# Kernel optimization log

Hardware: AMD Instinct MI355X
Metric: run time of the kernel (lower is better)

Reference implementation:

```python
import jax, jax.numpy as jnp
import numpy as np

B, S, D, H = 4, 2048, 128, 8

def setup_inputs() -> dict:
    key = jax.random.key(0)
    ks = jax.random.split(key, 11)
    sc_in = 1.0 / np.sqrt(D)
    sc_out = 1.0 / np.sqrt(H * D)
    return {
        "Q": jax.random.normal(ks[0], (B, S, D), jnp.float32),
        "K": jax.random.normal(ks[1], (B, S, D), jnp.float32),
        "V": jax.random.normal(ks[2], (B, S, D), jnp.float32),
        "WQ_w": jax.random.normal(ks[3], (H * D, D), jnp.float32) * sc_in,
        "WQ_b": jax.random.normal(ks[4], (H * D,), jnp.float32) * 0.01,
        "WK_w": jax.random.normal(ks[5], (H * D, D), jnp.float32) * sc_in,
        "WK_b": jax.random.normal(ks[6], (H * D,), jnp.float32) * 0.01,
        "WV_w": jax.random.normal(ks[7], (H * D, D), jnp.float32) * sc_in,
        "WV_b": jax.random.normal(ks[8], (H * D,), jnp.float32) * 0.01,
        "W_w": jax.random.normal(ks[9], (D, H * D), jnp.float32) * sc_out,
        "W_b": jax.random.normal(ks[10], (D,), jnp.float32) * 0.01,
    }

def reference(Q, K, V, WQ_w, WQ_b, WK_w, WK_b, WV_w, WV_b, W_w, W_b):
    b, s, d = Q.shape
    h = WQ_w.shape[0] // d
    # Linear projections: [b,s,d] -> [b,s,h*d] -> [b,h,s,d]
    rQ = (Q @ WQ_w.T + WQ_b).reshape(b, s, h, d).transpose(0, 2, 1, 3)
    rK = (K @ WK_w.T + WK_b).reshape(b, s, h, d).transpose(0, 2, 1, 3)
    rV = (V @ WV_w.T + WV_b).reshape(b, s, h, d).transpose(0, 2, 1, 3)
    # Scores: [b,h,s,s], scaled by sqrt(head_dim) = sqrt(input_dim)
    scores = jnp.einsum("bhqd,bhkd->bhqk", rQ, rK) / jnp.sqrt(jnp.asarray(d, rQ.dtype))
    sim = jax.nn.softmax(scores, axis=-1)
    # Attend and merge heads: [b,h,s,d] -> [b,s,h*d]
    oV = jnp.einsum("bhqk,bhkd->bqhd", sim, rV).reshape(b, s, h * d)
    return oV @ W_w.T + W_b
```

## Files before the change

### kernel.cpp

```cpp
#include <hip/hip_runtime.h>
#include <hip/hip_bf16.h>

typedef unsigned short u16;
typedef unsigned int   u32;
typedef short v8s __attribute__((ext_vector_type(8)));
typedef float v4f __attribute__((ext_vector_type(4)));
typedef float v16f __attribute__((ext_vector_type(16)));
typedef int   v2i __attribute__((ext_vector_type(2)));

#define MFMA16(a,b,c) __builtin_amdgcn_mfma_f32_16x16x32_bf16(a,b,c,0,0,0)
#define MFMA32(a,b,c) __builtin_amdgcn_mfma_f32_32x32x16_bf16(a,b,c,0,0,0)


__device__ __forceinline__ u16 f2b(float f){ u32 i; __builtin_memcpy(&i,&f,4); u32 r = (i + 0x7FFFu + ((i>>16)&1u))>>16; return (u16)r; }
__device__ __forceinline__ u32 pk2(float a, float b){
  __hip_bfloat162 h = __float22bfloat162_rn(make_float2(a,b));
  u32 r; __builtin_memcpy(&r,&h,4); return r;
}

__device__ __forceinline__ void gl16(const void* g, void* l){
  __builtin_amdgcn_global_load_lds((const __attribute__((address_space(1))) u32*)g,
                                   (__attribute__((address_space(3))) u32*)l, 16, 0, 0);
}

__device__ __forceinline__ void stage8f(const float* g, u16* l){
  float4 a = *(const float4*)g, b = *(const float4*)(g+4);
  uint4 q;
  q.x = pk2(a.x, a.y); q.y = pk2(a.z, a.w);
  q.z = pk2(b.x, b.y); q.w = pk2(b.z, b.w);
  *(uint4*)l = q;
}

__global__ __launch_bounds__(256) void proj_qkv(
    const float* __restrict__ Qx, const float* __restrict__ Kx, const float* __restrict__ Vx,
    const float* __restrict__ WQw, const float* __restrict__ WQb,
    const float* __restrict__ WKw, const float* __restrict__ WKb,
    const float* __restrict__ WVw, const float* __restrict__ WVb,
    u16* __restrict__ Qp, u16* __restrict__ Kp, u16* __restrict__ Vt)
{
  __shared__ u16 smem[32768];
  u16* As = smem;
  u16* Ws = smem + 16384;

  const int z = blockIdx.z;
  const float* X    = (z==0) ? Qx  : (z==1 ? Kx  : Vx);
  const float* W    = (z==0) ? WQw : (z==1 ? WKw : WVw);
  const float* bias = (z==0) ? WQb : (z==1 ? WKb : WVb);
  u16* out          = (z==0) ? Qp  : (z==1 ? Kp  : Vt);
  const float qs    = (z==0) ? 0.12751743076f : 1.0f;

  const int tid = threadIdx.x, wv = tid>>6, lane = tid&63;
  const int quad = lane>>4, l16 = lane&15;
  const int r4 = lane>>2, c4 = lane&3;
  const int m0 = blockIdx.x*128, n0 = blockIdx.y*128;

  for (int idx = wv; idx < 32; idx += 4) {
    int kt = idx >> 3, rg = idx & 7;
    int row = rg*16 + r4;
    stage8f(X + (size_t)(m0+row)*128 + kt*32 + c4*8, &As[kt*4096 + rg*512 + lane*8]);
    stage8f(W + (size_t)(n0+row)*128 + kt*32 + c4*8, &Ws[kt*4096 + rg*512 + lane*8]);
  }
  __syncthreads();

  const int wm = wv & 1, wn = wv >> 1;
  v4f acc[4][4];
#pragma unroll
  for (int i=0;i<4;i++)
#pragma unroll
    for (int j=0;j<4;j++) acc[i][j] = (v4f){0.f,0.f,0.f,0.f};

  if (z < 2) {
#pragma unroll
    for (int ks=0; ks<4; ++ks) {
      v8s af[4], bf[4];
#pragma unroll
      for (int mi=0; mi<4; ++mi) af[mi] = *(const v8s*)&As[ks*4096 + (wm*64+mi*16+l16)*32 + quad*8];
#pragma unroll
      for (int ni=0; ni<4; ++ni) bf[ni] = *(const v8s*)&Ws[ks*4096 + (wn*64+ni*16+l16)*32 + quad*8];
#pragma unroll
      for (int mi=0; mi<4; ++mi)
#pragma unroll
        for (int ni=0; ni<4; ++ni)
          acc[mi][ni] = MFMA16(bf[ni], af[mi], acc[mi][ni]);
    }
#pragma unroll
    for (int ni=0; ni<4; ++ni) {
      int nb = n0 + wn*64 + ni*16 + quad*4;
      float bv0 = bias[nb+0]*qs;
      float bv1 = bias[nb+1]*qs;
      float bv2 = bias[nb+2]*qs;
      float bv3 = bias[nb+3]*qs;
      int h = n0 >> 7, dh = nb & 127;
#pragma unroll
      for (int mi=0; mi<4; ++mi) {
        int m = m0 + wm*64 + mi*16 + l16;
        int b = m >> 11, s = m & 2047;
        uint2 pk;
        pk.x = pk2(fmaf(acc[mi][ni][0], qs, bv0), fmaf(acc[mi][ni][1], qs, bv1));
        pk.y = pk2(fmaf(acc[mi][ni][2], qs, bv2), fmaf(acc[mi][ni][3], qs, bv3));
        *(uint2*)&out[(size_t)(((b<<3) + h)*2048 + s)*128 + dh] = pk;
      }
    }
  } else {
#pragma unroll
    for (int ks=0; ks<4; ++ks) {
      v8s af[4], bf[4];
#pragma unroll
      for (int mi=0; mi<4; ++mi) af[mi] = *(const v8s*)&As[ks*4096 + (wm*64+mi*16+l16)*32 + quad*8];
#pragma unroll
      for (int ni=0; ni<4; ++ni) bf[ni] = *(const v8s*)&Ws[ks*4096 + (wn*64+ni*16+l16)*32 + quad*8];
#pragma unroll
      for (int mi=0; mi<4; ++mi)
#pragma unroll
        for (int ni=0; ni<4; ++ni)
          acc[mi][ni] = MFMA16(af[mi], bf[ni], acc[mi][ni]);
    }
    __syncthreads();
    u16* Cs = smem;
#pragma unroll
    for (int ni=0; ni<4; ++ni) {
      int nl = wn*64 + ni*16 + l16;
      float bv = bias[n0 + nl];
#pragma unroll
      for (int mi=0; mi<4; ++mi) {
        int ml = wm*64 + mi*16 + quad*4;
        uint2 pk;
        pk.x = pk2(acc[mi][ni][0] + bv, acc[mi][ni][1] + bv);
        pk.y = pk2(acc[mi][ni][2] + bv, acc[mi][ni][3] + bv);
        *(uint2*)&Cs[nl*136 + ml] = pk;
      }
    }
    __syncthreads();
    const int nl = tid >> 1;
    const int mb = (tid & 1) * 64;
    const int h = (n0 + nl) >> 7, dh = (n0 + nl) & 127;
    const int b = m0 >> 11, s0 = m0 & 2047;
    size_t gbase = (((size_t)((b<<3) + h)*128 + dh)*2048) + s0 + mb;
    size_t lbase = (size_t)nl*136 + mb;
#pragma unroll
    for (int j = 0; j < 8; ++j)
      *(uint4*)&out[gbase + j*8] = *(const uint4*)&Cs[lbase + j*8];
  }
}

__global__ __launch_bounds__(128, 2) void attn(
    const u16* __restrict__ Qp, const u16* __restrict__ Kp,
    const u16* __restrict__ Vt, u16* __restrict__ O)
{
  __shared__ u16 smem[16384];

  const int tid = threadIdx.x, wv = tid>>6, lane = tid&63;
  const int l32 = lane&31, h = lane>>5;

  const int n  = blockIdx.x;
  const int bh = (n&7)*4 + (n>>8);
  const int q0 = ((n>>3)&31) * 64;

  const u16* Qb = Qp + (size_t)bh*262144 + (size_t)q0*128;
  const u16* Kb = Kp + (size_t)bh*262144;
  const u16* Vb = Vt + (size_t)bh*262144;

  for (int r = 0; r < 8; ++r) {
    int idx = r*128 + tid;
    int kd = idx>>7, q = (idx>>1)&63, hh = idx&1;
    gl16(Qb + q*128 + kd*16 + hh*8, &smem[idx*8]);
  }
  __syncthreads();
  const int qrow = wv*32 + l32;
  v8s qf[8];
#pragma unroll
  for (int kd = 0; kd < 8; ++kd)
    qf[kd] = *(const v8s*)&smem[kd*1024 + qrow*16 + h*8];
  __syncthreads();

  int gK[4], gV[4], lK[4], lV[4];
#pragma unroll
  for (int r = 0; r < 4; ++r) {
    int idx = r*128 + tid;
    lK[r] = idx*8;  lV[r] = 8192 + idx*8;
    int key = idx>>4, pcK = idx&15;
    gK[r] = key*128 + (pcK ^ (key&15))*8;
    int d = idx>>2, pcV = idx&3;
    gV[r] = d*2048 + (pcV ^ ((d>>1)&3))*8;
  }
  int kfo[8], vfo[2];
#pragma unroll
  for (int kd = 0; kd < 8; ++kd) kfo[kd] = ((kd*2 + h) ^ (l32 & 15)) * 8;
#pragma unroll
  for (int kt = 0; kt < 2; ++kt) vfo[kt] = ((kt*2 + h) ^ ((l32>>1) & 3)) * 8;

  v8s onesf;
#pragma unroll
  for (int j = 0; j < 8; ++j) onesf[j] = (short)0x3F80;

  v16f oacc[4], lacc;
#pragma unroll
  for (int nt = 0; nt < 4; ++nt)
#pragma unroll
    for (int j = 0; j < 16; ++j) oacc[nt][j] = 0.f;
#pragma unroll
  for (int j = 0; j < 16; ++j) lacc[j] = 0.f;

#pragma unroll
  for (int r = 0; r < 4; ++r) gl16(Kb + gK[r], &smem[lK[r]]);
#pragma unroll
  for (int r = 0; r < 4; ++r) gl16(Vb + gV[r], &smem[lV[r]]);

  for (int it = 0; it < 64; ++it) {
    const int cur = it & 1;
    const int ko = cur*4096;
    const int vo = 8192 + cur*4096;
    __syncthreads();

    if (it + 1 < 64) {
      const u16* Kt  = Kb + (it+1)*4096;
      const u16* Vtt = Vb + (it+1)*32;
      const int po = (cur^1)*4096;
#pragma unroll
      for (int r = 0; r < 4; ++r) gl16(Kt  + gK[r], &smem[po + lK[r]]);
#pragma unroll
      for (int r = 0; r < 4; ++r) gl16(Vtt + gV[r], &smem[po + lV[r]]);
    }

    v16f sa;
#pragma unroll
    for (int j = 0; j < 16; ++j) sa[j] = 0.f;
    __builtin_amdgcn_s_setprio(1);
#pragma unroll
    for (int kd = 0; kd < 8; ++kd) {
      v8s kf = *(const v8s*)&smem[ko + l32*128 + kfo[kd]];
      sa = MFMA32(kf, qf[kd], sa);
    }
    __builtin_amdgcn_s_setprio(0);

    u32 P32[4][2];
#pragma unroll
    for (int g = 0; g < 4; ++g) {
      P32[g][0] = pk2(__builtin_amdgcn_exp2f(sa[g*4+0]),
                      __builtin_amdgcn_exp2f(sa[g*4+1]));
      P32[g][1] = pk2(__builtin_amdgcn_exp2f(sa[g*4+2]),
                      __builtin_amdgcn_exp2f(sa[g*4+3]));
    }

    v8s pf[2];
#pragma unroll
    for (int kt = 0; kt < 2; ++kt) {
      const int e = kt*2, o = e + 1;
      union { u32 u[4]; v8s s; } f;
#if __has_builtin(__builtin_amdgcn_permlane32_swap)
      v2i r0 = __builtin_amdgcn_permlane32_swap((int)P32[e][0], (int)P32[o][0], false, false);
      v2i r1 = __builtin_amdgcn_permlane32_swap((int)P32[e][1], (int)P32[o][1], false, false);
      f.u[0] = (u32)r0[0]; f.u[1] = (u32)r1[0];
      f.u[2] = (u32)r0[1]; f.u[3] = (u32)r1[1];
#else
      u32 a0 = P32[e][0], b0 = P32[o][0];
      u32 a1 = P32[e][1], b1 = P32[o][1];
      asm("v_permlane32_swap_b32 %0, %1" : "+v"(a0), "+v"(b0));
      asm("v_permlane32_swap_b32 %0, %1" : "+v"(a1), "+v"(b1));
      f.u[0] = a0; f.u[1] = a1; f.u[2] = b0; f.u[3] = b1;
#endif
      pf[kt] = f.s;
    }

    __builtin_amdgcn_s_setprio(1);
#pragma unroll
    for (int kt = 0; kt < 2; ++kt) {
      lacc = MFMA32(pf[kt], onesf, lacc);
#pragma unroll
      for (int nt = 0; nt < 4; ++nt) {
        v8s vf = *(const v8s*)&smem[vo + (nt*32 + l32)*32 + vfo[kt]];
        oacc[nt] = MFMA32(pf[kt], vf, oacc[nt]);
      }
    }
    __builtin_amdgcn_s_setprio(0);
  }

  const int b = bh >> 3, hd = bh & 7;
#pragma unroll
  for (int reg = 0; reg < 16; ++reg) {
    int q = q0 + wv*32 + (reg&3) + 8*(reg>>2) + 4*h;
    float inv = 1.0f / lacc[reg];
    size_t base = ((size_t)(b*2048 + q))*1024 + hd*128;
#pragma unroll
    for (int nt = 0; nt < 4; ++nt)
      O[base + nt*32 + l32] = f2b(oacc[nt][reg] * inv);
  }
}

__global__ __launch_bounds__(256) void outproj(
    const u16* __restrict__ A, const float* __restrict__ Ww,
    const float* __restrict__ Wb, float* __restrict__ out)
{
  __shared__ u16 As[2][2048];
  __shared__ u16 Ws[2][8192];

  const int tid = threadIdx.x, wv = tid>>6, lane = tid&63;
  const int quad = lane>>4, l16 = lane&15;
  const int r4 = lane>>2, c4 = lane&3;
  const int m0 = blockIdx.x*32;

  v4f acc[2][2];
#pragma unroll
  for (int i=0;i<2;i++)
#pragma unroll
    for (int j=0;j<2;j++) acc[i][j] = (v4f){0.f,0.f,0.f,0.f};

  auto stage = [&](int kb, int buf) {
    {
      int kt = wv >> 1, rg = wv & 1;
      int row = rg*16 + r4;
      gl16(A + (size_t)(m0+row)*1024 + kb + kt*32 + c4*8, &As[buf][kt*1024 + rg*512 + lane*8]);
    }
    for (int idx = wv; idx < 16; idx += 4) {
      int kt = idx >> 3, rg = idx & 7;
      int row = rg*16 + r4;
      stage8f(Ww + (size_t)row*1024 + kb + kt*32 + c4*8, &Ws[buf][kt*4096 + rg*512 + lane*8]);
    }
  };

  stage(0, 0);
  for (int kb = 0; kb < 1024; kb += 64) {
    const int cur = (kb >> 6) & 1;
    __syncthreads();
    if (kb + 64 < 1024) stage(kb + 64, cur ^ 1);
#pragma unroll
    for (int ks = 0; ks < 2; ++ks) {
      v8s af0 = *(const v8s*)&As[cur][ks*1024 + (l16)*32 + quad*8];
      v8s af1 = *(const v8s*)&As[cur][ks*1024 + (16 + l16)*32 + quad*8];
#pragma unroll
      for (int nj = 0; nj < 2; ++nj) {
        v8s bf = *(const v8s*)&Ws[cur][ks*4096 + ((wv*2+nj)*16 + l16)*32 + quad*8];
        acc[0][nj] = MFMA16(af0, bf, acc[0][nj]);
        acc[1][nj] = MFMA16(af1, bf, acc[1][nj]);
      }
    }
  }

#pragma unroll
  for (int nj = 0; nj < 2; ++nj) {
    int col = (wv*2+nj)*16 + l16;
    float bv = Wb[col];
#pragma unroll
    for (int mi = 0; mi < 2; ++mi) {
#pragma unroll
      for (int r = 0; r < 4; ++r) {
        int row = m0 + mi*16 + quad*4 + r;
        out[(size_t)row*128 + col] = acc[mi][nj][r] + bv;
      }
    }
  }
}

extern "C" void kernel_launch(void* const* d_in, const int* in_sizes, int n_in,
                              void* d_out, int out_size, void* d_ws, size_t ws_size,
                              hipStream_t stream) {
  const float* Q   = (const float*)d_in[0];
  const float* K   = (const float*)d_in[1];
  const float* V   = (const float*)d_in[2];
  const float* WQw = (const float*)d_in[3];
  const float* WQb = (const float*)d_in[4];
  const float* WKw = (const float*)d_in[5];
  const float* WKb = (const float*)d_in[6];
  const float* WVw = (const float*)d_in[7];
  const float* WVb = (const float*)d_in[8];
  const float* Ww  = (const float*)d_in[9];
  const float* Wb  = (const float*)d_in[10];
  u16* ws = (u16*)d_ws;

  const size_t SZ = (size_t)4*8*2048*128;
  u16* Qp = ws;
  u16* Kp = Qp + SZ;
  u16* Vt = Kp + SZ;
  u16* Ow = Vt + SZ;

  hipLaunchKernelGGL(proj_qkv, dim3(64,8,3), dim3(256), 0, stream,
                     Q,K,V,WQw,WQb,WKw,WKb,WVw,WVb,Qp,Kp,Vt);
  hipLaunchKernelGGL(attn, dim3(1024), dim3(128), 0, stream, Qp,Kp,Vt,Ow);
  hipLaunchKernelGGL(outproj, dim3(256), dim3(256), 0, stream, Ow, Ww, Wb, (float*)d_out);
}
```

Before: 223.9 us.

## Split attention key range across wave groups with 128-query blocks and reduce

The attention kernel now uses 512-thread blocks covering 128 queries. Four query waves are each paired with two key-split waves, and each iteration processes 64 keys. Every K/V tile loaded into shared memory is therefore reused by more waves, and the grid is halved. Partial output and row-sum accumulators from the second key half are reduced through shared memory before normalisation. The cost is more shared memory, extra syncs for the reduction, and fewer blocks per CU.

```diff
diff --git a/kernel.cpp b/kernel.cpp
--- a/kernel.cpp
+++ b/kernel.cpp
@@ -143,51 +143,54 @@
   }
 }
 
-__global__ __launch_bounds__(128, 2) void attn(
+__global__ __launch_bounds__(512, 4) void attn(
     const u16* __restrict__ Qp, const u16* __restrict__ Kp,
     const u16* __restrict__ Vt, u16* __restrict__ O)
 {
-  __shared__ u16 smem[16384];
+  __shared__ u16 smem[32768];
 
   const int tid = threadIdx.x, wv = tid>>6, lane = tid&63;
   const int l32 = lane&31, h = lane>>5;
+  const int qw = wv & 3, kw = wv >> 2;
 
   const int n  = blockIdx.x;
-  const int bh = (n&7)*4 + (n>>8);
-  const int q0 = ((n>>3)&31) * 64;
+  const int bh = (n&7)*4 + (n>>7);
+  const int q0 = ((n>>3)&15) * 128;
 
   const u16* Qb = Qp + (size_t)bh*262144 + (size_t)q0*128;
   const u16* Kb = Kp + (size_t)bh*262144;
   const u16* Vb = Vt + (size_t)bh*262144;
 
-  for (int r = 0; r < 8; ++r) {
-    int idx = r*128 + tid;
-    int kd = idx>>7, q = (idx>>1)&63, hh = idx&1;
+  for (int r = 0; r < 4; ++r) {
+    int idx = r*512 + tid;
+    int kd = idx>>8, q = (idx>>1)&127, hh = idx&1;
     gl16(Qb + q*128 + kd*16 + hh*8, &smem[idx*8]);
   }
   __syncthreads();
-  const int qrow = wv*32 + l32;
+  const int qrow = qw*32 + l32;
   v8s qf[8];
 #pragma unroll
   for (int kd = 0; kd < 8; ++kd)
-    qf[kd] = *(const v8s*)&smem[kd*1024 + qrow*16 + h*8];
+    qf[kd] = *(const v8s*)&smem[kd*2048 + qrow*16 + h*8];
   __syncthreads();
 
-  int gK[4], gV[4], lK[4], lV[4];
-#pragma unroll
-  for (int r = 0; r < 4; ++r) {
-    int idx = r*128 + tid;
-    lK[r] = idx*8;  lV[r] = 8192 + idx*8;
+  int gK[2], gV[2], lK[2], lV[2];
+#pragma unroll
+  for (int r = 0; r < 2; ++r) {
+    int idx = r*512 + tid;
+    lK[r] = idx*8;  lV[r] = 16384 + idx*8;
     int key = idx>>4, pcK = idx&15;
     gK[r] = key*128 + (pcK ^ (key&15))*8;
-    int d = idx>>2, pcV = idx&3;
-    gV[r] = d*2048 + (pcV ^ ((d>>1)&3))*8;
+    int d = idx>>3, pcV = idx&7;
+    gV[r] = d*2048 + (pcV ^ (d&7))*8;
   }
   int kfo[8], vfo[2];
 #pragma unroll
   for (int kd = 0; kd < 8; ++kd) kfo[kd] = ((kd*2 + h) ^ (l32 & 15)) * 8;
 #pragma unroll
-  for (int kt = 0; kt < 2; ++kt) vfo[kt] = ((kt*2 + h) ^ ((l32>>1) & 3)) * 8;
+  for (int kt = 0; kt < 2; ++kt) vfo[kt] = ((kw*4 + kt*2 + h) ^ (l32 & 7)) * 8;
+
+  const int krow = (kw*32 + l32) * 128;
 
   v8s onesf;
 #pragma unroll
@@ -202,24 +205,24 @@
   for (int j = 0; j < 16; ++j) lacc[j] = 0.f;
 
 #pragma unroll
-  for (int r = 0; r < 4; ++r) gl16(Kb + gK[r], &smem[lK[r]]);
-#pragma unroll
-  for (int r = 0; r < 4; ++r) gl16(Vb + gV[r], &smem[lV[r]]);
-
-  for (int it = 0; it < 64; ++it) {
+  for (int r = 0; r < 2; ++r) gl16(Kb + gK[r], &smem[lK[r]]);
+#pragma unroll
+  for (int r = 0; r < 2; ++r) gl16(Vb + gV[r], &smem[lV[r]]);
+
+  for (int it = 0; it < 32; ++it) {
     const int cur = it & 1;
-    const int ko = cur*4096;
-    const int vo = 8192 + cur*4096;
+    const int ko = cur*8192;
+    const int vo = 16384 + cur*8192;
     __syncthreads();
 
-    if (it + 1 < 64) {
-      const u16* Kt  = Kb + (it+1)*4096;
-      const u16* Vtt = Vb + (it+1)*32;
-      const int po = (cur^1)*4096;
-#pragma unroll
-      for (int r = 0; r < 4; ++r) gl16(Kt  + gK[r], &smem[po + lK[r]]);
-#pragma unroll
-      for (int r = 0; r < 4; ++r) gl16(Vtt + gV[r], &smem[po + lV[r]]);
+    if (it + 1 < 32) {
+      const u16* Kt  = Kb + (it+1)*8192;
+      const u16* Vtt = Vb + (it+1)*64;
+      const int po = (cur^1)*8192;
+#pragma unroll
+      for (int r = 0; r < 2; ++r) gl16(Kt  + gK[r], &smem[po + lK[r]]);
+#pragma unroll
+      for (int r = 0; r < 2; ++r) gl16(Vtt + gV[r], &smem[po + lV[r]]);
     }
 
     v16f sa;
@@ -228,7 +231,7 @@
     __builtin_amdgcn_s_setprio(1);
 #pragma unroll
     for (int kd = 0; kd < 8; ++kd) {
-      v8s kf = *(const v8s*)&smem[ko + l32*128 + kfo[kd]];
+      v8s kf = *(const v8s*)&smem[ko + krow + kfo[kd]];
       sa = MFMA32(kf, qf[kd], sa);
     }
     __builtin_amdgcn_s_setprio(0);
@@ -268,22 +271,54 @@
       lacc = MFMA32(pf[kt], onesf, lacc);
 #pragma unroll
       for (int nt = 0; nt < 4; ++nt) {
-        v8s vf = *(const v8s*)&smem[vo + (nt*32 + l32)*32 + vfo[kt]];
+        v8s vf = *(const v8s*)&smem[vo + (nt*32 + l32)*64 + vfo[kt]];
         oacc[nt] = MFMA32(pf[kt], vf, oacc[nt]);
       }
     }
     __builtin_amdgcn_s_setprio(0);
   }
 
-  const int b = bh >> 3, hd = bh & 7;
-#pragma unroll
-  for (int reg = 0; reg < 16; ++reg) {
-    int q = q0 + wv*32 + (reg&3) + 8*(reg>>2) + 4*h;
-    float inv = 1.0f / lacc[reg];
-    size_t base = ((size_t)(b*2048 + q))*1024 + hd*128;
-#pragma unroll
-    for (int nt = 0; nt < 4; ++nt)
-      O[base + nt*32 + l32] = f2b(oacc[nt][reg] * inv);
+  {
+    float* red = (float*)smem;
+    for (int round = 0; round < 2; ++round) {
+      __syncthreads();
+      if ((qw >> 1) == round && kw == 1) {
+        const int base = (qw & 1) * 5120;
+#pragma unroll
+        for (int reg = 0; reg < 16; ++reg) {
+          int row = (reg&3) + 8*(reg>>2) + 4*h;
+#pragma unroll
+          for (int nt = 0; nt < 4; ++nt)
+            red[base + row*160 + nt*32 + l32] = oacc[nt][reg];
+          red[base + row*160 + 128 + l32] = lacc[reg];
+        }
+      }
+      __syncthreads();
+      if ((qw >> 1) == round && kw == 0) {
+        const int base = (qw & 1) * 5120;
+#pragma unroll
+        for (int reg = 0; reg < 16; ++reg) {
+          int row = (reg&3) + 8*(reg>>2) + 4*h;
+#pragma unroll
+          for (int nt = 0; nt < 4; ++nt)
+            oacc[nt][reg] += red[base + row*160 + nt*32 + l32];
+          lacc[reg] += red[base + row*160 + 128 + l32];
+        }
+      }
+    }
+  }
+
+  if (kw == 0) {
+    const int b = bh >> 3, hd = bh & 7;
+#pragma unroll
+    for (int reg = 0; reg < 16; ++reg) {
+      int q = q0 + qw*32 + (reg&3) + 8*(reg>>2) + 4*h;
+      float inv = 1.0f / lacc[reg];
+      size_t base = ((size_t)(b*2048 + q))*1024 + hd*128;
+#pragma unroll
+      for (int nt = 0; nt < 4; ++nt)
+        O[base + nt*32 + l32] = f2b(oacc[nt][reg] * inv);
+    }
   }
 }
 
@@ -375,6 +410,6 @@
 
   hipLaunchKernelGGL(proj_qkv, dim3(64,8,3), dim3(256), 0, stream,
                      Q,K,V,WQw,WQb,WKw,WKb,WVw,WVb,Qp,Kp,Vt);
-  hipLaunchKernelGGL(attn, dim3(1024), dim3(128), 0, stream, Qp,Kp,Vt,Ow);
+  hipLaunchKernelGGL(attn, dim3(512), dim3(512), 0, stream, Qp,Kp,Vt,Ow);
   hipLaunchKernelGGL(outproj, dim3(256), dim3(256), 0, stream, Ow, Ww, Wb, (float*)d_out);
 }
```

New measurement: 332.9 us. 1.49x slower.
